# Performance work log

Measured on AMD Instinct MI355X. Metric: run time of the kernel, lower is better.

The kernel has to match this reference:

```python
import jax, jax.numpy as jnp
import numpy as np

D = 128
NODE_COUNTS = (200000, 3000, 20000)  # operation, machine, job
E = 500000
EDGE_TYPES = [(s, t) for s in range(3) for t in range(3)]  # itertools.product order
BN_EPS = 1e-5


def setup_inputs() -> dict:
    key = jax.random.key(0)
    ks = jax.random.split(key, 40)
    x_operation = jax.random.normal(ks[0], (NODE_COUNTS[0], D), dtype=jnp.float32)
    x_machine = jax.random.normal(ks[1], (NODE_COUNTS[1], D), dtype=jnp.float32)
    x_job = jax.random.normal(ks[2], (NODE_COUNTS[2], D), dtype=jnp.float32)
    # edge_index[k] = [src_idx, dst_idx] for edge type k=(s,t)
    eis = []
    for k, (s, t) in enumerate(EDGE_TYPES):
        src = jax.random.randint(ks[3 + 2 * k], (E,), 0, NODE_COUNTS[s], dtype=jnp.int32)
        dst = jax.random.randint(ks[4 + 2 * k], (E,), 0, NODE_COUNTS[t], dtype=jnp.int32)
        eis.append(jnp.stack([src, dst]))
    edge_index = jnp.stack(eis)  # [9, 2, E]
    scale = 1.0 / np.sqrt(D)
    W1 = jax.random.normal(ks[30], (3, D, D), dtype=jnp.float32) * scale
    b1 = jnp.zeros((3, D), dtype=jnp.float32)
    g1 = jnp.ones((3, D), dtype=jnp.float32)
    be1 = jnp.zeros((3, D), dtype=jnp.float32)
    W2 = jax.random.normal(ks[31], (3, D, D), dtype=jnp.float32) * scale
    b2 = jnp.zeros((3, D), dtype=jnp.float32)
    g2 = jnp.ones((3, D), dtype=jnp.float32)
    be2 = jnp.zeros((3, D), dtype=jnp.float32)
    eps = jnp.zeros((9,), dtype=jnp.float32)  # GINConv train_eps init 0 per edge type
    return {"x_operation": x_operation, "x_machine": x_machine, "x_job": x_job,
            "edge_index": edge_index, "W1": W1, "b1": b1, "g1": g1, "be1": be1,
            "W2": W2, "b2": b2, "g2": g2, "be2": be2, "eps": eps}


def _bn(h, gamma, beta):
    # BatchNorm1d in training mode: batch stats, biased variance
    mean = h.mean(axis=0)
    var = h.var(axis=0)
    return (h - mean) * jax.lax.rsqrt(var + BN_EPS) * gamma + beta


def reference(x_operation, x_machine, x_job, edge_index, W1, b1, g1, be1, W2, b2, g2, be2, eps):
    xs = [x_operation, x_machine, x_job]

    def mlp(h, i):
        h = jax.nn.relu(_bn(h @ W1[i] + b1[i], g1[i], be1[i]))
        h = jax.nn.relu(_bn(h @ W2[i] + b2[i], g2[i], be2[i]))
        return h

    outs = [jnp.zeros((n, D), dtype=jnp.float32) for n in NODE_COUNTS]
    for k, (s, t) in enumerate(EDGE_TYPES):
        src, dst = edge_index[k, 0], edge_index[k, 1]
        # gather source features along edges, scatter-add into destinations
        agg = jax.ops.segment_sum(xs[s][src], dst, num_segments=NODE_COUNTS[t])
        h = mlp((1.0 + eps[k]) * xs[t] + agg, s)  # GINConv: nn keyed by SOURCE type
        outs[t] = outs[t] + h  # HeteroConv aggr='sum' per destination type
    return jnp.concatenate(outs, axis=0)  # [sum(NODE_COUNTS), D]
```

## Files before the change

kernel.cpp:

```cpp
#include <hip/hip_runtime.h>
#include <hip/hip_fp16.h>

#define D 128
#define E_PER 500000
#define TOT_ROWS 669000
#define CH 4096
#define NR64 64
#define SLABSZ ((size_t)223000 * 256)

typedef _Float16 f16;
typedef _Float16 f16x8 __attribute__((ext_vector_type(8)));
typedef _Float16 f16x4 __attribute__((ext_vector_type(4)));
typedef _Float16 f16x2 __attribute__((ext_vector_type(2)));
typedef float f32x4 __attribute__((ext_vector_type(4)));

__device__ const int d_SEGB[9] = {0, 200000, 203000, 223000, 423000, 426000,
                                  446000, 646000, 649000};
__device__ const int d_XB[3] = {0, 200000, 203000};
__device__ const int d_NC[3] = {200000, 3000, 20000};
__device__ const int d_T64LO[3] = {0, 3125, 3172};
__device__ const int d_T64HI[3] = {3125, 3172, 3485};

__device__ __forceinline__ unsigned a_swz(int row, int byteoff) {
    return (unsigned)(row * 256 + byteoff) ^ (unsigned)((row & 7) << 4);
}

__device__ __forceinline__ void tile_map64(int g, int& t, int& tl) {
    if (g < 3125)      { t = 0; tl = g; }
    else if (g < 3172) { t = 1; tl = g - 3125; }
    else               { t = 2; tl = g - 3172; }
}

__global__ void precast(const float* __restrict__ W1,
                        const float* __restrict__ W2,
                        f16* __restrict__ Wth) {
    int i = blockIdx.x * 256 + threadIdx.x;
    if (i >= 2 * 3 * 128 * 128) return;
    int layer = i / 49152;
    int rem = i - layer * 49152;
    int s = rem / 16384;
    int r2 = rem & 16383;
    int kk = r2 >> 7;
    int c  = r2 & 127;
    const float* W = layer ? W2 : W1;
    Wth[(((size_t)layer * 3 + s) * 128 + c) * 128 + kk] = (f16)W[((size_t)s * 128 + kk) * 128 + c];
}

__global__ void cast16_all(const float* __restrict__ x0,
                           const float* __restrict__ x1,
                           const float* __restrict__ x2,
                           f16* __restrict__ y) {
    const int total = 223000 * 16;
    for (int i = blockIdx.x * 256 + threadIdx.x; i < total; i += gridDim.x * 256) {
        int row = i >> 4, c8 = i & 15;
        const float* src;
        if (row < 200000)      src = x0 + (size_t)row * D;
        else if (row < 203000) src = x1 + (size_t)(row - 200000) * D;
        else                   src = x2 + (size_t)(row - 203000) * D;
        f32x4 v0 = ((const f32x4*)src)[c8 * 2];
        f32x4 v1 = ((const f32x4*)src)[c8 * 2 + 1];
        f16x8 h;
        #pragma unroll
        for (int j = 0; j < 4; ++j) { h[j] = (f16)v0[j]; h[4 + j] = (f16)v1[j]; }
        ((f16x8*)(y + (size_t)row * D))[c8] = h;
    }
}

__global__ __launch_bounds__(256) void bucket_count(const int* __restrict__ ei,
                                                    int* __restrict__ bcnt) {
    __shared__ int hist[256];
    int k = blockIdx.y, tid = threadIdx.x;
    const int* dstp = ei + (size_t)k * 2 * E_PER + E_PER;
    unsigned Nt = (unsigned)d_NC[k % 3];
    int base = blockIdx.x * CH;
    int hi = min(base + CH, E_PER);
    hist[tid] = 0;
    __syncthreads();
    for (int i = base + tid; i < hi; i += 256) {
        unsigned b = ((unsigned)dstp[i] << 8) / Nt;
        atomicAdd(&hist[b], 1);
    }
    __syncthreads();
    if (hist[tid]) atomicAdd(&bcnt[k * 256 + tid], hist[tid]);
}

__global__ void bucket_scan(const int* __restrict__ bcnt,
                            int* __restrict__ bbase, int* __restrict__ bcursor) {
    __shared__ int sb[256];
    int t = threadIdx.x;
    int loc[9];
    int s = 0;
    #pragma unroll
    for (int j = 0; j < 9; ++j) { loc[j] = bcnt[t * 9 + j]; s += loc[j]; }
    sb[t] = s; __syncthreads();
    int v = s;
    for (int off = 1; off < 256; off <<= 1) {
        int u = (t >= off) ? sb[t - off] : 0;
        __syncthreads();
        sb[t] += u;
        __syncthreads();
    }
    int pre = sb[t] - v;
    #pragma unroll
    for (int j = 0; j < 9; ++j) {
        bbase[t * 9 + j] = pre;
        bcursor[t * 9 + j] = pre;
        pre += loc[j];
    }
    if (t == 255) bbase[2304] = pre;
}

__global__ __launch_bounds__(256) void bin_scatter(const int* __restrict__ ei,
                                                   int* __restrict__ bcursor,
                                                   int2* __restrict__ binned) {
    __shared__ int hist[256], gb[256], cur[256];
    int k = blockIdx.y, tid = threadIdx.x;
    const int* srcp = ei + (size_t)k * 2 * E_PER;
    const int* dstp = srcp + E_PER;
    unsigned Nt = (unsigned)d_NC[k % 3];
    int base = blockIdx.x * CH;
    int hi = min(base + CH, E_PER);
    hist[tid] = 0;
    __syncthreads();
    for (int i = base + tid; i < hi; i += 256) {
        unsigned b = ((unsigned)dstp[i] << 8) / Nt;
        atomicAdd(&hist[b], 1);
    }
    __syncthreads();
    gb[tid] = hist[tid] ? atomicAdd(&bcursor[k * 256 + tid], hist[tid]) : 0;
    cur[tid] = 0;
    __syncthreads();
    for (int i = base + tid; i < hi; i += 256) {
        int src = srcp[i], dst = dstp[i];
        unsigned b = ((unsigned)dst << 8) / Nt;
        int r = atomicAdd(&cur[b], 1);
        binned[(size_t)gb[b] + r] = make_int2(src, dst);
    }
}

__global__ __launch_bounds__(256) void fine_fill(const int2* __restrict__ binned,
                                                 const int* __restrict__ bbase,
                                                 int* __restrict__ rowstart,
                                                 int* __restrict__ ssrc) {
    __shared__ int rcnt[784];
    __shared__ int excl[784];
    __shared__ int scur[784];
    __shared__ int sb[256];
    int k = blockIdx.y, b = blockIdx.x, tid = threadIdx.x;
    int Nt = d_NC[k % 3];
    int segb = d_SEGB[k];
    int row_lo = (b * Nt + 255) >> 8;
    int row_hi = ((b + 1) * Nt + 255) >> 8;
    int nrows = row_hi - row_lo;
    int ebase = bbase[k * 256 + b];
    int eend  = bbase[k * 256 + b + 1];
    for (int i = tid; i < nrows; i += 256) rcnt[i] = 0;
    __syncthreads();
    for (int e = ebase + tid; e < eend; e += 256)
        atomicAdd(&rcnt[binned[e].y - row_lo], 1);
    __syncthreads();
    int stride = (nrows + 255) >> 8;
    int lo = tid * stride;
    int hi2 = min(lo + stride, nrows);
    int s = 0;
    for (int i = lo; i < hi2; ++i) s += rcnt[i];
    sb[tid] = s; __syncthreads();
    int v = s;
    for (int off = 1; off < 256; off <<= 1) {
        int u = (tid >= off) ? sb[tid - off] : 0;
        __syncthreads();
        sb[tid] += u;
        __syncthreads();
    }
    int pre = sb[tid] - v;
    for (int i = lo; i < hi2; ++i) {
        excl[i] = pre;
        scur[i] = pre;
        pre += rcnt[i];
    }
    __syncthreads();
    for (int i = tid; i < nrows; i += 256)
        rowstart[segb + row_lo + i] = ebase + excl[i];
    if (k == 8 && b == 255 && tid == 0) rowstart[TOT_ROWS] = eend;
    for (int e = ebase + tid; e < eend; e += 256) {
        int2 ed = binned[e];
        int r = atomicAdd(&scur[ed.y - row_lo], 1);
        ssrc[ebase + r] = ed.x;
    }
}

__global__ __launch_bounds__(256) void aggregate_t1(const f16* __restrict__ x16,
                                                    const int* __restrict__ rowstart,
                                                    const int* __restrict__ ssrc,
                                                    char* __restrict__ slabs,
                                                    const float* __restrict__ eps9) {
    __shared__ float part[4][128];
    int row = blockIdx.x;
    int s = blockIdx.y;
    int k = s * 3 + 1;
    const int* rs = rowstart + d_SEGB[k];
    const f16* xsrc = x16 + (size_t)d_XB[s] * D;
    const f16* xt   = x16 + (size_t)d_XB[1] * D;
    char* slab = slabs + (size_t)s * SLABSZ + (size_t)d_XB[1] * 256;
    float epsv = 1.0f + eps9[k];
    int tid  = threadIdx.x;
    int lane = tid & 63;
    int w    = tid >> 6;
    int grp  = lane >> 4;
    int cs   = lane & 15;
    int estart = w * 4 + grp, estep = 16;
    float acc[8];
    #pragma unroll
    for (int j = 0; j < 8; ++j) acc[j] = 0.f;
    int e1 = rs[row + 1];
    int e  = rs[row] + estart;
    for (; e + 3 * estep < e1; e += 4 * estep) {
        int s0 = ssrc[e], s1 = ssrc[e + estep], s2 = ssrc[e + 2 * estep], s3 = ssrc[e + 3 * estep];
        f16x8 v0 = ((const f16x8*)(xsrc + (size_t)s0 * D))[cs];
        f16x8 v1 = ((const f16x8*)(xsrc + (size_t)s1 * D))[cs];
        f16x8 v2 = ((const f16x8*)(xsrc + (size_t)s2 * D))[cs];
        f16x8 v3 = ((const f16x8*)(xsrc + (size_t)s3 * D))[cs];
        #pragma unroll
        for (int j = 0; j < 8; ++j)
            acc[j] += ((float)v0[j] + (float)v1[j]) + ((float)v2[j] + (float)v3[j]);
    }
    for (; e < e1; e += estep) {
        int s0 = ssrc[e];
        f16x8 v0 = ((const f16x8*)(xsrc + (size_t)s0 * D))[cs];
        #pragma unroll
        for (int j = 0; j < 8; ++j) acc[j] += (float)v0[j];
    }
    #pragma unroll
    for (int j = 0; j < 8; ++j) {
        acc[j] += __shfl_xor(acc[j], 16);
        acc[j] += __shfl_xor(acc[j], 32);
    }
    if (lane < 16) {
        #pragma unroll
        for (int j = 0; j < 8; ++j) part[w][cs * 8 + j] = acc[j];
    }
    __syncthreads();
    if (w == 0 && lane < 16) {
        f16x8 xv = ((const f16x8*)(xt + (size_t)row * D))[cs];
        f16x8 h;
        #pragma unroll
        for (int j = 0; j < 8; ++j) {
            float v = (part[0][cs*8+j] + part[1][cs*8+j]) + (part[2][cs*8+j] + part[3][cs*8+j]);
            h[j] = (f16)(v + epsv * (float)xv[j]);
        }
        ((f16x8*)(slab + (size_t)row * 256))[cs] = h;
    }
}

__global__ __launch_bounds__(256) void gemm_l1f(char* __restrict__ slabs,
                                                const f16* __restrict__ x16,
                                                const int* __restrict__ rowstart,
                                                const int* __restrict__ ssrc,
                                                const f16* __restrict__ Wth,
                                                const float* __restrict__ b1,
                                                const float* __restrict__ eps9,
                                                float* __restrict__ partials) {
    __shared__ alignas(16) char atile[64 * 256];
    __shared__ float wst[4][256];
    const int tid  = threadIdx.x;
    const int lane = tid & 63;
    const int w    = tid >> 6;
    const int s    = blockIdx.y;
    int t, tl;
    tile_map64(blockIdx.x, t, tl);
    const int N = d_NC[t];
    const int row0 = tl * 64;
    const int k = s * 3 + t;
    char* slab = slabs + (size_t)s * SLABSZ + (size_t)d_XB[t] * 256;

    if (t != 1) {
        const f16* xsrc = x16 + (size_t)d_XB[s] * D;
        const f16* xt   = x16 + (size_t)d_XB[t] * D;
        const int* rs = rowstart + d_SEGB[k];
        float epsv = 1.0f + eps9[k];
        int grp = tid >> 4, cs = tid & 15;
        for (int i = 0; i < 4; ++i) {
            int r = i * 16 + grp;
            int row = row0 + r;
            f16x8 h = {0, 0, 0, 0, 0, 0, 0, 0};
            if (row < N) {
                f16x8 xv = ((const f16x8*)(xt + (size_t)row * D))[cs];
                float acc[8];
                #pragma unroll
                for (int j = 0; j < 8; ++j) acc[j] = epsv * (float)xv[j];
                int e = rs[row], e1 = rs[row + 1];
                for (; e + 3 < e1; e += 4) {
                    int s0 = ssrc[e], s1 = ssrc[e + 1], s2 = ssrc[e + 2], s3 = ssrc[e + 3];
                    f16x8 v0 = ((const f16x8*)(xsrc + (size_t)s0 * D))[cs];
                    f16x8 v1 = ((const f16x8*)(xsrc + (size_t)s1 * D))[cs];
                    f16x8 v2 = ((const f16x8*)(xsrc + (size_t)s2 * D))[cs];
                    f16x8 v3 = ((const f16x8*)(xsrc + (size_t)s3 * D))[cs];
                    #pragma unroll
                    for (int j = 0; j < 8; ++j)
                        acc[j] += ((float)v0[j] + (float)v1[j]) + ((float)v2[j] + (float)v3[j]);
                }
                if (e + 1 < e1) {
                    int s0 = ssrc[e], s1 = ssrc[e + 1];
                    f16x8 v0 = ((const f16x8*)(xsrc + (size_t)s0 * D))[cs];
                    f16x8 v1 = ((const f16x8*)(xsrc + (size_t)s1 * D))[cs];
                    #pragma unroll
                    for (int j = 0; j < 8; ++j) acc[j] += (float)v0[j] + (float)v1[j];
                    e += 2;
                }
                if (e < e1) {
                    int s0 = ssrc[e];
                    f16x8 v0 = ((const f16x8*)(xsrc + (size_t)s0 * D))[cs];
                    #pragma unroll
                    for (int j = 0; j < 8; ++j) acc[j] += (float)v0[j];
                }
                #pragma unroll
                for (int j = 0; j < 8; ++j) h[j] = (f16)acc[j];
            }
            *(f16x8*)(atile + a_swz(r, cs * 16)) = h;
        }
    } else {
        #pragma unroll
        for (int p = 0; p < 4; ++p) {
            int r  = p * 16 + (tid >> 4);
            int c8 = tid & 15;
            int row = row0 + r;
            if (row >= N) row = N - 1;
            const char* src = slab + (size_t)row * 256 + (unsigned)((c8 * 16) ^ ((r & 7) << 4));
            __builtin_amdgcn_global_load_lds(
                (const __attribute__((address_space(1))) void*)src,
                (__attribute__((address_space(3))) void*)(atile + p * 4096 + w * 1024),
                16, 0, 0);
        }
    }
    __syncthreads();

    const f16* Wt = Wth + (size_t)s * 16384;
    f32x4 acc0[8];
    #pragma unroll
    for (int ct = 0; ct < 8; ++ct) acc0[ct] = (f32x4){0.f, 0.f, 0.f, 0.f};
    const int arow = (w << 4) + (lane & 15);
    const int kq = (lane >> 4) * 8;
    #pragma unroll
    for (int ks = 0; ks < 4; ++ks) {
        f16x8 af = *(const f16x8*)(atile + a_swz(arow, (ks * 32 + kq) * 2));
        #pragma unroll
        for (int ct = 0; ct < 8; ++ct) {
            f16x8 bf = *(const f16x8*)(Wt + (size_t)(ct * 16 + (lane & 15)) * D + ks * 32 + kq);
            acc0[ct] = __builtin_amdgcn_mfma_f32_16x16x32_f16(af, bf, acc0[ct], 0, 0, 0);
        }
    }

    const int col_lo = lane & 15;
    const int lrb0 = (w << 4) + ((lane >> 4) << 2);
    #pragma unroll
    for (int ct = 0; ct < 8; ++ct) {
        int col = ct * 16 + col_lo;
        float bv = b1[s * D + col];
        float s_ = 0.f, q_ = 0.f;
        #pragma unroll
        for (int r = 0; r < 4; ++r) {
            int lrow = lrb0 + r;
            float val = acc0[ct][r] + bv;
            if (row0 + lrow < N) { s_ += val; q_ += val * val; }
            *(f16*)(atile + a_swz(lrow, col * 2)) = (f16)val;
        }
        s_ += __shfl_xor(s_, 16); q_ += __shfl_xor(q_, 16);
        s_ += __shfl_xor(s_, 32); q_ += __shfl_xor(q_, 32);
        if (lane < 16) { wst[w][col] = s_; wst[w][128 + col] = q_; }
    }
    __syncthreads();

    #pragma unroll
    for (int p = 0; p < 4; ++p) {
        int r  = p * 16 + (tid >> 4);
        int c8 = tid & 15;
        int row = row0 + r;
        if (row < N)
            *(f16x8*)(slab + (size_t)row * 256 + c8 * 16) = *(const f16x8*)(atile + a_swz(r, c8 * 16));
    }
    float pv = wst[0][tid] + wst[1][tid] + wst[2][tid] + wst[3][tid];
    partials[((size_t)blockIdx.x * 3 + s) * 256 + tid] = pv;
}

__global__ __launch_bounds__(256) void gemm_l2(char* __restrict__ slabs,
                                               const f16* __restrict__ Wth2,
                                               const float* __restrict__ bias,
                                               const float* __restrict__ affa,
                                               const float* __restrict__ affc,
                                               float* __restrict__ partials) {
    __shared__ alignas(16) char atile[64 * 256];
    __shared__ float wst[4][256];
    const int tid  = threadIdx.x;
    const int lane = tid & 63;
    const int w    = tid >> 6;
    const int s    = blockIdx.y;
    int t, tl;
    tile_map64(blockIdx.x, t, tl);
    const int N = d_NC[t];
    const int row0 = tl * 64;
    const int k = s * 3 + t;
    char* slab = slabs + (size_t)s * SLABSZ + (size_t)d_XB[t] * 256;
    const int c8 = tid & 15;

    f32x4 a0 = ((const f32x4*)(affa + k * 128))[c8 * 2];
    f32x4 a1 = ((const f32x4*)(affa + k * 128))[c8 * 2 + 1];
    f32x4 c0 = ((const f32x4*)(affc + k * 128))[c8 * 2];
    f32x4 c1 = ((const f32x4*)(affc + k * 128))[c8 * 2 + 1];

    f16x8 zv[4];
    #pragma unroll
    for (int p = 0; p < 4; ++p) {
        int r = p * 16 + (tid >> 4);
        int row = row0 + r;
        zv[p] = (row < N) ? ((const f16x8*)(slab + (size_t)row * 256))[c8]
                          : (f16x8){0, 0, 0, 0, 0, 0, 0, 0};
    }
    #pragma unroll
    for (int p = 0; p < 4; ++p) {
        int r = p * 16 + (tid >> 4);
        f16x8 hv;
        #pragma unroll
        for (int j = 0; j < 4; ++j) {
            float t0 = (float)zv[p][j] * a0[j] + c0[j];
            float t1 = (float)zv[p][4 + j] * a1[j] + c1[j];
            hv[j]     = (f16)(t0 > 0.f ? t0 : 0.f);
            hv[4 + j] = (f16)(t1 > 0.f ? t1 : 0.f);
        }
        *(f16x8*)(atile + a_swz(r, c8 * 16)) = hv;
    }
    __syncthreads();

    const f16* Wt = Wth2 + (size_t)s * 16384;
    f32x4 acc0[8];
    #pragma unroll
    for (int ct = 0; ct < 8; ++ct) acc0[ct] = (f32x4){0.f, 0.f, 0.f, 0.f};
    const int arow = (w << 4) + (lane & 15);
    const int kq = (lane >> 4) * 8;
    #pragma unroll
    for (int ks = 0; ks < 4; ++ks) {
        f16x8 af = *(const f16x8*)(atile + a_swz(arow, (ks * 32 + kq) * 2));
        #pragma unroll
        for (int ct = 0; ct < 8; ++ct) {
            f16x8 bf = *(const f16x8*)(Wt + (size_t)(ct * 16 + (lane & 15)) * D + ks * 32 + kq);
            acc0[ct] = __builtin_amdgcn_mfma_f32_16x16x32_f16(af, bf, acc0[ct], 0, 0, 0);
        }
    }

    const int col_lo = lane & 15;
    const int lrb0 = (w << 4) + ((lane >> 4) << 2);
    #pragma unroll
    for (int ct = 0; ct < 8; ++ct) {
        int col = ct * 16 + col_lo;
        float bv = bias[s * D + col];
        float s_ = 0.f, q_ = 0.f;
        #pragma unroll
        for (int r = 0; r < 4; ++r) {
            int lrow = lrb0 + r;
            float val = acc0[ct][r] + bv;
            if (row0 + lrow < N) { s_ += val; q_ += val * val; }
            *(f16*)(atile + a_swz(lrow, col * 2)) = (f16)val;
        }
        s_ += __shfl_xor(s_, 16); q_ += __shfl_xor(q_, 16);
        s_ += __shfl_xor(s_, 32); q_ += __shfl_xor(q_, 32);
        if (lane < 16) { wst[w][col] = s_; wst[w][128 + col] = q_; }
    }
    __syncthreads();

    #pragma unroll
    for (int p = 0; p < 4; ++p) {
        int r = p * 16 + (tid >> 4);
        int row = row0 + r;
        if (row < N)
            *(f16x8*)(slab + (size_t)row * 256 + c8 * 16) = *(const f16x8*)(atile + a_swz(r, c8 * 16));
    }
    float pv = wst[0][tid] + wst[1][tid] + wst[2][tid] + wst[3][tid];
    partials[((size_t)blockIdx.x * 3 + s) * 256 + tid] = pv;
}

__global__ void bn_reduce(const float* __restrict__ partials,
                          float* __restrict__ partial2) {
    int k = blockIdx.y, tid = threadIdx.x;
    int s = k / 3, t = k % 3;
    int lo = d_T64LO[t], hi = d_T64HI[t];
    float v = 0.f;
    for (int b = lo + blockIdx.x; b < hi; b += NR64)
        v += partials[((size_t)b * 3 + s) * 256 + tid];
    partial2[((size_t)k * NR64 + blockIdx.x) * 256 + tid] = v;
}

__global__ void bn_params(const float* __restrict__ partial2,
                          const float* __restrict__ g, const float* __restrict__ be,
                          float* __restrict__ affa, float* __restrict__ affc) {
    __shared__ float red[256];
    int k = blockIdx.x, tid = threadIdx.x;
    int s = k / 3, t = k % 3;
    float v = 0.f;
    #pragma unroll 4
    for (int b = 0; b < NR64; ++b)
        v += partial2[((size_t)k * NR64 + b) * 256 + tid];
    red[tid] = v;
    __syncthreads();
    if (tid < 128) {
        float sm = red[tid], q = red[128 + tid];
        float n = (float)d_NC[t];
        float mean = sm / n;
        float var  = q / n - mean * mean;
        float a = g[s * D + tid] * rsqrtf(var + 1e-5f);
        affa[k * 128 + tid] = a;
        affc[k * 128 + tid] = be[s * D + tid] - mean * a;
    }
}

__global__ __launch_bounds__(256) void accum_all(const char* __restrict__ slabs,
                                                 const float* __restrict__ affa,
                                                 const float* __restrict__ affc,
                                                 float* __restrict__ outp) {
    const int total = 223000 * 16;
    for (int i = blockIdx.x * 256 + threadIdx.x; i < total; i += gridDim.x * 256) {
        int row = i >> 4;
        int c8  = i & 15;
        int t = (row < 200000) ? 0 : (row < 203000) ? 1 : 2;
        f32x4 o0 = {0.f, 0.f, 0.f, 0.f}, o1 = {0.f, 0.f, 0.f, 0.f};
        #pragma unroll
        for (int s = 0; s < 3; ++s) {
            int k = s * 3 + t;
            f16x8 z = ((const f16x8*)(slabs + (size_t)s * SLABSZ + (size_t)row * 256))[c8];
            f32x4 a0 = ((const f32x4*)(affa + k * 128))[c8 * 2];
            f32x4 a1 = ((const f32x4*)(affa + k * 128))[c8 * 2 + 1];
            f32x4 c0 = ((const f32x4*)(affc + k * 128))[c8 * 2];
            f32x4 c1 = ((const f32x4*)(affc + k * 128))[c8 * 2 + 1];
            #pragma unroll
            for (int j = 0; j < 4; ++j) {
                float t0 = (float)z[j] * a0[j] + c0[j];
                float t1 = (float)z[4 + j] * a1[j] + c1[j];
                o0[j] += t0 > 0.f ? t0 : 0.f;
                o1[j] += t1 > 0.f ? t1 : 0.f;
            }
        }
        ((f32x4*)(outp + (size_t)row * D))[c8 * 2]     = o0;
        ((f32x4*)(outp + (size_t)row * D))[c8 * 2 + 1] = o1;
    }
}

extern "C" void kernel_launch(void* const* d_in, const int* in_sizes, int n_in,
                              void* d_out, int out_size, void* d_ws, size_t ws_size,
                              hipStream_t stream) {
    const float* x0  = (const float*)d_in[0];
    const float* x1  = (const float*)d_in[1];
    const float* x2  = (const float*)d_in[2];
    const int*   ei  = (const int*)d_in[3];
    const float* W1  = (const float*)d_in[4];
    const float* b1  = (const float*)d_in[5];
    const float* g1  = (const float*)d_in[6];
    const float* be1 = (const float*)d_in[7];
    const float* W2  = (const float*)d_in[8];
    const float* b2  = (const float*)d_in[9];
    const float* g2  = (const float*)d_in[10];
    const float* be2 = (const float*)d_in[11];
    const float* eps9 = (const float*)d_in[12];
    float* outp = (float*)d_out;

    char* ws = (char*)d_ws;
    size_t off = 0;
    char* slabs = ws;                 off += 3 * SLABSZ;
    int2* binned = (int2*)slabs;
    f16* x16    = (f16*)(ws + off);   off += SLABSZ;
    int* ssrc   = (int*)(ws + off);   off += (size_t)9 * E_PER * 4;
    int* rowstart = (int*)(ws + off); off += (size_t)(TOT_ROWS + 2) * 4;
    off = (off + 255) & ~(size_t)255;
    int* bcnt   = (int*)(ws + off);   off += 2308 * 4;
    int* bbase  = (int*)(ws + off);   off += 2308 * 4;
    int* bcursor= (int*)(ws + off);   off += 2308 * 4;
    off = (off + 255) & ~(size_t)255;
    float* partials = (float*)(ws + off); off += (size_t)3485 * 3 * 256 * 4;
    float* partial2 = (float*)(ws + off); off += (size_t)9 * NR64 * 256 * 4;
    float* aff1a = (float*)(ws + off); off += 9 * 128 * 4;
    float* aff1c = (float*)(ws + off); off += 9 * 128 * 4;
    float* aff2a = (float*)(ws + off); off += 9 * 128 * 4;
    float* aff2c = (float*)(ws + off); off += 9 * 128 * 4;
    f16* Wth = (f16*)(ws + off); off += (size_t)2 * 3 * 128 * 128 * sizeof(f16);

    precast<<<384, 256, 0, stream>>>(W1, W2, Wth);
    cast16_all<<<2048, 256, 0, stream>>>(x0, x1, x2, x16);

    hipMemsetAsync(bcnt, 0, 2308 * 4, stream);
    int nchunk = (E_PER + CH - 1) / CH;
    bucket_count<<<dim3(nchunk, 9), 256, 0, stream>>>(ei, bcnt);
    bucket_scan<<<1, 256, 0, stream>>>(bcnt, bbase, bcursor);
    bin_scatter<<<dim3(nchunk, 9), 256, 0, stream>>>(ei, bcursor, binned);
    fine_fill<<<dim3(256, 9), 256, 0, stream>>>(binned, bbase, rowstart, ssrc);

    aggregate_t1<<<dim3(3000, 3), 256, 0, stream>>>(x16, rowstart, ssrc, slabs, eps9);

    gemm_l1f<<<dim3(3485, 3), 256, 0, stream>>>(slabs, x16, rowstart, ssrc,
                                                Wth, b1, eps9, partials);
    bn_reduce<<<dim3(NR64, 9), 256, 0, stream>>>(partials, partial2);
    bn_params<<<9, 256, 0, stream>>>(partial2, g1, be1, aff1a, aff1c);

    gemm_l2<<<dim3(3485, 3), 256, 0, stream>>>(slabs, Wth + 3 * 16384, b2,
                                               aff1a, aff1c, partials);
    bn_reduce<<<dim3(NR64, 9), 256, 0, stream>>>(partials, partial2);
    bn_params<<<9, 256, 0, stream>>>(partial2, g2, be2, aff2a, aff2c);

    accum_all<<<4096, 256, 0, stream>>>(slabs, aff2a, aff2c, outp);
}
```

Measured before the change: 786.0 us.

## Use padded fixed-width neighbor lists for operation-destination aggregation

Adds an 8-slot padded source-index table for destination type operation, filled during fine_fill, with empty slots pointing at an appended zero row in the f16 feature buffer. The layer-1 GEMM gather for t==0 then issues all eight neighbor loads unconditionally, with no data-dependent loop, so more loads are in flight at once. Rows with more than eight edges fall back to the CSR list. Row bounds are also staged in shared memory for the t==0 and t==2 paths. The cost is an extra init kernel, about 19 MB of extra index traffic, and wasted loads of the zero row for low-degree nodes.

```diff
diff --git a/kernel.cpp b/kernel.cpp
--- a/kernel.cpp
+++ b/kernel.cpp
@@ -6,6 +6,7 @@
 #define TOT_ROWS 669000
 #define CH 4096
 #define NR64 64
+#define ZROW 223000
 #define SLABSZ ((size_t)223000 * 256)
 
 typedef _Float16 f16;
@@ -50,20 +51,28 @@
                            const float* __restrict__ x1,
                            const float* __restrict__ x2,
                            f16* __restrict__ y) {
-    const int total = 223000 * 16;
+    const int total = 223001 * 16;
     for (int i = blockIdx.x * 256 + threadIdx.x; i < total; i += gridDim.x * 256) {
         int row = i >> 4, c8 = i & 15;
-        const float* src;
-        if (row < 200000)      src = x0 + (size_t)row * D;
-        else if (row < 203000) src = x1 + (size_t)(row - 200000) * D;
-        else                   src = x2 + (size_t)(row - 203000) * D;
-        f32x4 v0 = ((const f32x4*)src)[c8 * 2];
-        f32x4 v1 = ((const f32x4*)src)[c8 * 2 + 1];
-        f16x8 h;
-        #pragma unroll
-        for (int j = 0; j < 4; ++j) { h[j] = (f16)v0[j]; h[4 + j] = (f16)v1[j]; }
+        f16x8 h = {0, 0, 0, 0, 0, 0, 0, 0};
+        if (row < ZROW) {
+            const float* src;
+            if (row < 200000)      src = x0 + (size_t)row * D;
+            else if (row < 203000) src = x1 + (size_t)(row - 200000) * D;
+            else                   src = x2 + (size_t)(row - 203000) * D;
+            f32x4 v0 = ((const f32x4*)src)[c8 * 2];
+            f32x4 v1 = ((const f32x4*)src)[c8 * 2 + 1];
+            #pragma unroll
+            for (int j = 0; j < 4; ++j) { h[j] = (f16)v0[j]; h[4 + j] = (f16)v1[j]; }
+        }
         ((f16x8*)(y + (size_t)row * D))[c8] = h;
     }
+}
+
+__global__ void psrc_init(int* __restrict__ psrc) {
+    const int total = 3 * 200000 * 8;
+    for (int i = blockIdx.x * 256 + threadIdx.x; i < total; i += gridDim.x * 256)
+        psrc[i] = ZROW;
 }
 
 __global__ __launch_bounds__(256) void bucket_count(const int* __restrict__ ei,
@@ -141,7 +150,8 @@
 __global__ __launch_bounds__(256) void fine_fill(const int2* __restrict__ binned,
                                                  const int* __restrict__ bbase,
                                                  int* __restrict__ rowstart,
-                                                 int* __restrict__ ssrc) {
+                                                 int* __restrict__ ssrc,
+                                                 int* __restrict__ psrc) {
     __shared__ int rcnt[784];
     __shared__ int excl[784];
     __shared__ int scur[784];
@@ -182,10 +192,19 @@
     for (int i = tid; i < nrows; i += 256)
         rowstart[segb + row_lo + i] = ebase + excl[i];
     if (k == 8 && b == 255 && tid == 0) rowstart[TOT_ROWS] = eend;
+    const int is_t0 = ((k % 3) == 0);
+    const int sidx = k / 3;
+    const int xb = d_XB[sidx];
     for (int e = ebase + tid; e < eend; e += 256) {
         int2 ed = binned[e];
-        int r = atomicAdd(&scur[ed.y - row_lo], 1);
+        int lrow = ed.y - row_lo;
+        int r = atomicAdd(&scur[lrow], 1);
         ssrc[ebase + r] = ed.x;
+        if (is_t0) {
+            int j = r - excl[lrow];
+            if (j < 8)
+                psrc[((size_t)sidx * 200000 + ed.y) * 8 + j] = ed.x + xb;
+        }
     }
 }
 
@@ -256,12 +275,14 @@
                                                 const f16* __restrict__ x16,
                                                 const int* __restrict__ rowstart,
                                                 const int* __restrict__ ssrc,
+                                                const int* __restrict__ psrc,
                                                 const f16* __restrict__ Wth,
                                                 const float* __restrict__ b1,
                                                 const float* __restrict__ eps9,
                                                 float* __restrict__ partials) {
     __shared__ alignas(16) char atile[64 * 256];
     __shared__ float wst[4][256];
+    __shared__ int sbnd[65];
     const int tid  = threadIdx.x;
     const int lane = tid & 63;
     const int w    = tid >> 6;
@@ -273,22 +294,73 @@
     const int k = s * 3 + t;
     char* slab = slabs + (size_t)s * SLABSZ + (size_t)d_XB[t] * 256;
 
-    if (t != 1) {
+    if (t == 0) {
+        const f16* xsrc = x16 + (size_t)d_XB[s] * D;
+        const int* rs = rowstart + d_SEGB[k];
+        const float epsv = 1.0f + eps9[k];
+        const int grp = tid >> 4, cs = tid & 15;
+
+        if (tid <= 64) sbnd[tid] = rs[row0 + tid];
+        __syncthreads();
+
+        #pragma unroll
+        for (int i = 0; i < 4; ++i) {
+            int r = i * 16 + grp;
+            int row = row0 + r;
+            const int4* pp = (const int4*)(psrc + ((size_t)s * 200000 + row) * 8);
+            int4 pa = pp[0];
+            int4 pb = pp[1];
+            f16x8 xv = ((const f16x8*)(x16 + (size_t)row * D))[cs];
+            float acc[8];
+            #pragma unroll
+            for (int j = 0; j < 8; ++j) acc[j] = epsv * (float)xv[j];
+            f16x8 v0 = ((const f16x8*)(x16 + (size_t)pa.x * D))[cs];
+            f16x8 v1 = ((const f16x8*)(x16 + (size_t)pa.y * D))[cs];
+            f16x8 v2 = ((const f16x8*)(x16 + (size_t)pa.z * D))[cs];
+            f16x8 v3 = ((const f16x8*)(x16 + (size_t)pa.w * D))[cs];
+            f16x8 v4 = ((const f16x8*)(x16 + (size_t)pb.x * D))[cs];
+            f16x8 v5 = ((const f16x8*)(x16 + (size_t)pb.y * D))[cs];
+            f16x8 v6 = ((const f16x8*)(x16 + (size_t)pb.z * D))[cs];
+            f16x8 v7 = ((const f16x8*)(x16 + (size_t)pb.w * D))[cs];
+            #pragma unroll
+            for (int j = 0; j < 8; ++j)
+                acc[j] += (((float)v0[j] + (float)v1[j]) + ((float)v2[j] + (float)v3[j]))
+                        + (((float)v4[j] + (float)v5[j]) + ((float)v6[j] + (float)v7[j]));
+            int e0 = sbnd[r], e1 = sbnd[r + 1];
+            if (e1 - e0 > 8) {
+                for (int e = e0 + 8; e < e1; ++e) {
+                    int si = ssrc[e];
+                    f16x8 v = ((const f16x8*)(xsrc + (size_t)si * D))[cs];
+                    #pragma unroll
+                    for (int j = 0; j < 8; ++j) acc[j] += (float)v[j];
+                }
+            }
+            f16x8 h;
+            #pragma unroll
+            for (int j = 0; j < 8; ++j) h[j] = (f16)acc[j];
+            *(f16x8*)(atile + a_swz(r, cs * 16)) = h;
+        }
+    } else if (t == 2) {
         const f16* xsrc = x16 + (size_t)d_XB[s] * D;
         const f16* xt   = x16 + (size_t)d_XB[t] * D;
         const int* rs = rowstart + d_SEGB[k];
-        float epsv = 1.0f + eps9[k];
-        int grp = tid >> 4, cs = tid & 15;
+        const float epsv = 1.0f + eps9[k];
+        const int grp = tid >> 4, cs = tid & 15;
+        const int nrows_t = min(64, N - row0);
+
+        if (tid <= nrows_t) sbnd[tid] = rs[row0 + tid];
+        __syncthreads();
+
         for (int i = 0; i < 4; ++i) {
             int r = i * 16 + grp;
             int row = row0 + r;
             f16x8 h = {0, 0, 0, 0, 0, 0, 0, 0};
-            if (row < N) {
+            if (r < nrows_t) {
                 f16x8 xv = ((const f16x8*)(xt + (size_t)row * D))[cs];
                 float acc[8];
                 #pragma unroll
                 for (int j = 0; j < 8; ++j) acc[j] = epsv * (float)xv[j];
-                int e = rs[row], e1 = rs[row + 1];
+                int e = sbnd[r], e1 = sbnd[r + 1];
                 for (; e + 3 < e1; e += 4) {
                     int s0 = ssrc[e], s1 = ssrc[e + 1], s2 = ssrc[e + 2], s3 = ssrc[e + 3];
                     f16x8 v0 = ((const f16x8*)(xsrc + (size_t)s0 * D))[cs];
@@ -564,8 +636,9 @@
     size_t off = 0;
     char* slabs = ws;                 off += 3 * SLABSZ;
     int2* binned = (int2*)slabs;
-    f16* x16    = (f16*)(ws + off);   off += SLABSZ;
+    f16* x16    = (f16*)(ws + off);   off += SLABSZ + 256;
     int* ssrc   = (int*)(ws + off);   off += (size_t)9 * E_PER * 4;
+    int* psrc   = (int*)(ws + off);   off += (size_t)3 * 200000 * 8 * 4;
     int* rowstart = (int*)(ws + off); off += (size_t)(TOT_ROWS + 2) * 4;
     off = (off + 255) & ~(size_t)255;
     int* bcnt   = (int*)(ws + off);   off += 2308 * 4;
@@ -582,17 +655,18 @@
 
     precast<<<384, 256, 0, stream>>>(W1, W2, Wth);
     cast16_all<<<2048, 256, 0, stream>>>(x0, x1, x2, x16);
+    psrc_init<<<2048, 256, 0, stream>>>(psrc);
 
     hipMemsetAsync(bcnt, 0, 2308 * 4, stream);
     int nchunk = (E_PER + CH - 1) / CH;
     bucket_count<<<dim3(nchunk, 9), 256, 0, stream>>>(ei, bcnt);
     bucket_scan<<<1, 256, 0, stream>>>(bcnt, bbase, bcursor);
     bin_scatter<<<dim3(nchunk, 9), 256, 0, stream>>>(ei, bcursor, binned);
-    fine_fill<<<dim3(256, 9), 256, 0, stream>>>(binned, bbase, rowstart, ssrc);
+    fine_fill<<<dim3(256, 9), 256, 0, stream>>>(binned, bbase, rowstart, ssrc, psrc);
 
     aggregate_t1<<<dim3(3000, 3), 256, 0, stream>>>(x16, rowstart, ssrc, slabs, eps9);
 
-    gemm_l1f<<<dim3(3485, 3), 256, 0, stream>>>(slabs, x16, rowstart, ssrc,
+    gemm_l1f<<<dim3(3485, 3), 256, 0, stream>>>(slabs, x16, rowstart, ssrc, psrc,
                                                 Wth, b1, eps9, partials);
     bn_reduce<<<dim3(NR64, 9), 256, 0, stream>>>(partials, partial2);
     bn_params<<<9, 256, 0, stream>>>(partial2, g1, be1, aff1a, aff1c);
```

Result: slower. 805.3 us (+2.5%).
